# Optimization experiments

Hardware: AMD Instinct MI355X
Metric: run time of the kernel (lower is better)

The kernel has to match this reference:

```python
import jax, jax.numpy as jnp
import numpy as np

B, T, D = 4, 4096, 1024
H, HD = 16, 64
EPS = 1e-6


def setup_inputs() -> dict:
    key = jax.random.key(0)
    ks = jax.random.split(key, 5)
    scale = 1.0 / np.sqrt(D)
    return {
        "x": jax.random.normal(ks[0], (B, T, D), dtype=jnp.float32),
        "Wq": jax.random.normal(ks[1], (D, H * HD), dtype=jnp.float32) * scale,
        "Wk": jax.random.normal(ks[2], (D, H * HD), dtype=jnp.float32) * scale,
        "Wv": jax.random.normal(ks[3], (D, H * HD), dtype=jnp.float32) * scale,
        "Wo": jax.random.normal(ks[4], (H * HD, D), dtype=jnp.float32) * scale,
    }


def _feature_map(x):
    # ELU + 1 feature map (always positive)
    return jax.nn.elu(x) + 1.0


def _causal_linear_attention(q, k, v, eps=EPS):
    # q,k,v: (B,H,T,Dk/Dv) -> scan over T with running state
    Dk = q.shape[-1]
    Dv = v.shape[-1]
    qT = jnp.moveaxis(q, 2, 0)  # (T,B,H,Dk)
    kT = jnp.moveaxis(k, 2, 0)
    vT = jnp.moveaxis(v, 2, 0)

    S0 = jnp.zeros((q.shape[0], q.shape[1], Dk, Dv), dtype=q.dtype)
    z0 = jnp.zeros((q.shape[0], q.shape[1], Dk), dtype=q.dtype)

    def step(carry, qkv_t):
        S, z = carry
        q_t, k_t, v_t = qkv_t
        S = S + jnp.einsum('bhd,bhe->bhde', k_t, v_t)
        z = z + k_t
        num = jnp.einsum('bhd,bhde->bhe', q_t, S)
        den = jnp.einsum('bhd,bhd->bh', q_t, z) + eps
        return (S, z), num / den[..., None]

    _, yT = jax.lax.scan(step, (S0, z0), (qT, kT, vT))  # yT: (T,B,H,Dv)
    return jnp.moveaxis(yT, 0, 2)  # (B,H,T,Dv)


def reference(x, Wq, Wk, Wv, Wo):
    b, t, _ = x.shape

    def proj(W):
        return (x @ W).reshape(b, t, H, HD).transpose(0, 2, 1, 3)  # (B,H,T,HD)

    q = _feature_map(proj(Wq))
    k = _feature_map(proj(Wk))
    v = proj(Wv)
    y = _causal_linear_attention(q, k, v)  # (B,H,T,HD)
    y = y.transpose(0, 2, 1, 3).reshape(b, t, H * HD)
    return y @ Wo
```

## Files before the change

kernel.cpp:

```cpp
#include <hip/hip_runtime.h>


typedef __bf16 bf16;
typedef __bf16 bf16x4 __attribute__((ext_vector_type(4)));
typedef __bf16 bf16x8 __attribute__((ext_vector_type(8)));
typedef float f32x4 __attribute__((ext_vector_type(4)));

#define EPS 1e-6f

#define BAR() asm volatile("s_barrier" ::: "memory")
#define VMCNT4() asm volatile("s_waitcnt vmcnt(4)" ::: "memory")
#define VMCNT0() asm volatile("s_waitcnt vmcnt(0)" ::: "memory")

__device__ __forceinline__ void gl_lds16(const void* g, void* l) {
  __builtin_amdgcn_global_load_lds(
      (__attribute__((address_space(1))) void*)g,
      (__attribute__((address_space(3))) void*)l, 16, 0, 0);
}

__device__ __forceinline__ float fmact(float v) {
  return v > 0.f ? v + 1.f : __expf(v);
}

__global__ __launch_bounds__(256) void prep(const float* __restrict__ x,
                                            const float* __restrict__ Wq,
                                            const float* __restrict__ Wk,
                                            const float* __restrict__ Wv,
                                            const float* __restrict__ Wo,
                                            bf16* __restrict__ XB,
                                            bf16* __restrict__ WT3,
                                            bf16* __restrict__ WOT) {
  const int bid = blockIdx.x;
  const int t = threadIdx.x;
  if (bid < 8192) {
    size_t base = ((size_t)bid * 256 + t) * 8;
    float4 v0 = *(const float4*)&x[base];
    float4 v1 = *(const float4*)&x[base + 4];
    bf16x8 o;
    o[0] = (bf16)v0.x; o[1] = (bf16)v0.y; o[2] = (bf16)v0.z; o[3] = (bf16)v0.w;
    o[4] = (bf16)v1.x; o[5] = (bf16)v1.y; o[6] = (bf16)v1.z; o[7] = (bf16)v1.w;
    *(bf16x8*)&XB[base] = o;
    return;
  }
  __shared__ float tile[64][65];
  const int wi = (bid - 8192) >> 8;
  const int local = (bid - 8192) & 255;
  const float* W = (wi == 0) ? Wq : (wi == 1) ? Wk : (wi == 2) ? Wv : Wo;
  bf16* WT = (wi == 3) ? WOT : WT3 + (size_t)wi * 1048576;
  const int k0 = (local & 15) * 64, n0 = (local >> 4) * 64;
  {
    const int r4 = t / 16, c4 = (t % 16) * 4;
#pragma unroll
    for (int rr = 0; rr < 4; ++rr) {
      int r = r4 + rr * 16;
      float4 v = *(const float4*)&W[(size_t)(k0 + r) * 1024 + n0 + c4];
      tile[r][c4] = v.x; tile[r][c4 + 1] = v.y;
      tile[r][c4 + 2] = v.z; tile[r][c4 + 3] = v.w;
    }
  }
  __syncthreads();
  const int nl = t / 4, kb = (t % 4) * 16;
  bf16x8 o0, o1;
#pragma unroll
  for (int j = 0; j < 8; ++j) {
    o0[j] = (bf16)tile[kb + j][nl];
    o1[j] = (bf16)tile[kb + 8 + j][nl];
  }
  *(bf16x8*)&WT[(size_t)(n0 + nl) * 1024 + k0 + kb] = o0;
  *(bf16x8*)&WT[(size_t)(n0 + nl) * 1024 + k0 + kb + 8] = o1;
}

template <int PROJ>
__global__ __launch_bounds__(512, 2) void gemm8(const bf16* __restrict__ A,
                                                const bf16* __restrict__ BT,
                                                bf16* __restrict__ Obf,
                                                float* __restrict__ Of,
                                                const int N, const int gy) {
  extern __shared__ bf16 lds[];
  const int t = threadIdx.x;
  const int w = t >> 6, l = t & 63;
  const int nwg = (int)gridDim.x, cpx = nwg >> 3;
  const int f = ((int)blockIdx.x & 7) * cpx + ((int)blockIdx.x >> 3);
  const int bx = f / gy, by = f - bx * gy;
  const int m0 = bx * 256, n0 = by * 256;
  const int wm = (w >> 2) * 128, wn = (w & 3) * 64;
  const int lr = l & 15, lg = l >> 4;
  const int aslc = (w >> 2) * 8192;
  const int bslc = 16384 + ((w & 3) >> 1) * 8192;
  const int brow = (w & 1) * 64;
  const int srow = t >> 3;
  const int scol = ((t & 7) ^ ((t >> 3) & 7)) * 8;

  f32x4 acc[8][4] = {};
  bf16x8 bv[8];

#define FRAG(c, slc, sr_, ks_)                                          \
  (*(const bf16x8*)&lds[(c) * 32768 + (slc) + (sr_) * 64 +              \
                        (((ks_) * 32 + lg * 8) ^ (((sr_) & 7) << 3))])

#define STG(dbuf, slc, rbase, PTR, kt)                                        \
  do {                                                                        \
    const bf16* _s = (PTR) + (size_t)((rbase) + srow) * 1024 + (kt) * 64 + scol; \
    bf16* _d = lds + (dbuf) * 32768 + (slc) + w * 512;                        \
    gl_lds16(_s, _d);                                                         \
    gl_lds16(_s + 65536, _d + 4096);                                          \
  } while (0)

#define PHASE(c, q, STAGE_STMT, VM)                                           \
  {                                                                           \
    bf16x8 av[4];                                                             \
    _Pragma("unroll") for (int mi = 0; mi < 2; ++mi)                          \
      _Pragma("unroll") for (int kk = 0; kk < 2; ++kk)                        \
        av[mi * 2 + kk] = FRAG(c, aslc, (q) * 32 + mi * 16 + lr, kk);         \
    if ((q) == 0) {                                                           \
      _Pragma("unroll") for (int n = 0; n < 4; ++n)                           \
        _Pragma("unroll") for (int kk = 0; kk < 2; ++kk)                      \
          bv[n * 2 + kk] = FRAG(c, bslc, brow + n * 16 + lr, kk);             \
    }                                                                         \
    STAGE_STMT;                                                               \
    if (VM) VMCNT4();                                                         \
    BAR();                                                                    \
    __builtin_amdgcn_s_setprio(1);                                            \
    _Pragma("unroll") for (int mi = 0; mi < 2; ++mi)                          \
      _Pragma("unroll") for (int n = 0; n < 4; ++n)                           \
        _Pragma("unroll") for (int kk = 0; kk < 2; ++kk)                      \
          acc[(q) * 2 + mi][n] = __builtin_amdgcn_mfma_f32_16x16x32_bf16(     \
              av[mi * 2 + kk], bv[n * 2 + kk], acc[(q) * 2 + mi][n], 0, 0, 0);\
    __builtin_amdgcn_s_setprio(0);                                            \
    BAR();                                                                    \
  }

  STG(0, 0, m0, A, 0);        STG(0, 8192, m0 + 128, A, 0);
  STG(0, 16384, n0, BT, 0);   STG(0, 24576, n0 + 128, BT, 0);
  STG(1, 16384, n0, BT, 1);   STG(1, 24576, n0 + 128, BT, 1);
  VMCNT4();
  BAR();

#pragma unroll 1
  for (int I = 0; I < 8; ++I) {
    const int t2 = 2 * I;
    const int k1 = t2 + 1;
    const int k2 = (t2 + 2 > 15) ? 15 : t2 + 2;
    const int k3 = (t2 + 3 > 15) ? 15 : t2 + 3;
    PHASE(0, 0, STG(1, 0, m0, A, k1), 0);
    PHASE(0, 1, STG(1, 8192, m0 + 128, A, k1), 0);
    PHASE(0, 2, STG(0, 16384, n0, BT, k2), 0);
    PHASE(0, 3, STG(0, 24576, n0 + 128, BT, k2), 1);
    PHASE(1, 0, STG(0, 0, m0, A, k2), 0);
    PHASE(1, 1, STG(0, 8192, m0 + 128, A, k2), 0);
    PHASE(1, 2, STG(1, 16384, n0, BT, k3), 0);
    PHASE(1, 3, STG(1, 24576, n0 + 128, BT, k3), 1);
  }
  VMCNT0();
#undef PHASE
#undef STG
#undef FRAG
#pragma unroll
  for (int m = 0; m < 8; ++m)
#pragma unroll
    for (int n = 0; n < 4; ++n)
#pragma unroll
      for (int r = 0; r < 4; ++r) {
        int row = m0 + wm + m * 16 + lg * 4 + r;
        int col = n0 + wn + n * 16 + lr;
        float v = acc[m][n][r];
        if (PROJ) {
          if (col < 2048) v = fmact(v);
          Obf[(size_t)row * N + col] = (bf16)v;
        } else {
          Of[(size_t)row * N + col] = v;
        }
      }
}

__global__ __launch_bounds__(256) void chunk_ktv(const bf16* __restrict__ QKV,
                                                 float* __restrict__ S_ws,
                                                 float* __restrict__ z_ws) {
  const int blk = blockIdx.x;
  const int bh = blk >> 5, c = blk & 31;
  const int b = bh >> 4, h = bh & 15;
  const size_t rowbase = (size_t)b * 4096 + (size_t)c * 128;
  __shared__ alignas(16) bf16 KT[64 * 136];
  __shared__ alignas(16) bf16 VT[64 * 136];
  __shared__ float zpart[4][64];
  const int t = threadIdx.x;
  {
    const int r = t >> 1, c0 = (t & 1) * 32;
    const bf16* kp = QKV + (rowbase + r) * 3072 + 1024 + h * 64 + c0;
    const bf16* vp = QKV + (rowbase + r) * 3072 + 2048 + h * 64 + c0;
    bf16x8 kv[4], vv[4];
#pragma unroll
    for (int q8 = 0; q8 < 4; ++q8) {
      kv[q8] = *(const bf16x8*)&kp[q8 * 8];
      vv[q8] = *(const bf16x8*)&vp[q8 * 8];
    }
#pragma unroll
    for (int q8 = 0; q8 < 4; ++q8)
#pragma unroll
      for (int j = 0; j < 8; ++j) {
        KT[(c0 + q8 * 8 + j) * 136 + r] = kv[q8][j];
        VT[(c0 + q8 * 8 + j) * 136 + r] = vv[q8][j];
      }
  }
  __syncthreads();
  {
    const int d = t & 63, part = t >> 6;
    float zs = 0.f;
#pragma unroll
    for (int tt = 0; tt < 32; ++tt) zs += (float)KT[d * 136 + part * 32 + tt];
    zpart[part][d] = zs;
  }
  __syncthreads();
  if (t < 64)
    z_ws[(size_t)blk * 64 + t] =
        zpart[0][t] + zpart[1][t] + zpart[2][t] + zpart[3][t];
  const int l = t & 63, w = t >> 6;
  const int lr = l & 15, lg = l >> 4, lk = lg * 8;
  f32x4 acc[4] = {};
#pragma unroll
  for (int ks = 0; ks < 4; ++ks) {
    const int k0 = ks * 32;
    bf16x8 a = *(const bf16x8*)&VT[(w * 16 + lr) * 136 + k0 + lk];
#pragma unroll
    for (int n = 0; n < 4; ++n) {
      bf16x8 bk = *(const bf16x8*)&KT[(n * 16 + lr) * 136 + k0 + lk];
      acc[n] = __builtin_amdgcn_mfma_f32_16x16x32_bf16(a, bk, acc[n], 0, 0, 0);
    }
  }
#pragma unroll
  for (int n = 0; n < 4; ++n)
#pragma unroll
    for (int r = 0; r < 4; ++r) {
      int e = w * 16 + lg * 4 + r;
      int d = n * 16 + lr;
      S_ws[((size_t)blk * 64 + e) * 64 + d] = acc[n][r];
    }
}

__global__ __launch_bounds__(256) void prefix_scan(const float* __restrict__ S_ws,
                                                   const float* __restrict__ z_ws,
                                                   bf16* __restrict__ STp,
                                                   float* __restrict__ zP) {
  const int bh = blockIdx.x >> 2, dq = blockIdx.x & 3;
  const int t = threadIdx.x;
  const int e = t >> 2, d0 = dq * 16 + (t & 3) * 4;
  float r0 = 0.f, r1 = 0.f, r2 = 0.f, r3 = 0.f, zr = 0.f;
  const bool doz = (dq == 0) && (t < 64);
  const size_t base = (size_t)bh * 32;
  float4 v = *(const float4*)&S_ws[base * 4096 + e * 64 + d0];
  float zv = doz ? z_ws[base * 64 + t] : 0.f;
  for (int c = 0; c < 32; ++c) {
    float4 vn = {0.f, 0.f, 0.f, 0.f};
    float zn = 0.f;
    if (c < 31) {
      vn = *(const float4*)&S_ws[(base + c + 1) * 4096 + e * 64 + d0];
      if (doz) zn = z_ws[(base + c + 1) * 64 + t];
    }
    const size_t cb = base + c;
    bf16x4 o;
    o[0] = (bf16)r0; o[1] = (bf16)r1; o[2] = (bf16)r2; o[3] = (bf16)r3;
    *(bf16x4*)&STp[cb * 4096 + e * 64 + d0] = o;
    if (doz) zP[cb * 64 + t] = zr;
    r0 += v.x; r1 += v.y; r2 += v.z; r3 += v.w;
    zr += zv;
    v = vn; zv = zn;
  }
}

__global__ __launch_bounds__(256) void chunk_attn(const bf16* __restrict__ QKV,
                                                  const bf16* __restrict__ STp,
                                                  const float* __restrict__ zP,
                                                  bf16* __restrict__ Y) {
  const int blk = blockIdx.x;
  const int bh = blk >> 5, c = blk & 31;
  const int b = bh >> 4, h = bh & 15;
  const size_t cb = (size_t)bh * 32 + c;
  const size_t rowbase = (size_t)b * 4096 + (size_t)c * 128;
  const bf16* Q = QKV + rowbase * 3072 + h * 64;
  const bf16* K = QKV + rowbase * 3072 + 1024 + h * 64;
  const bf16* V = QKV + rowbase * 3072 + 2048 + h * 64;
  __shared__ alignas(16) bf16 VT[64 * 136];
  __shared__ alignas(16) bf16 P[128 * 136];
  __shared__ float den[128];
  const int t = threadIdx.x;
  {
    const int r = t >> 1, c0 = (t & 1) * 32;
    const bf16* vp = V + (size_t)r * 3072 + c0;
    bf16x8 vv[4];
#pragma unroll
    for (int q8 = 0; q8 < 4; ++q8) vv[q8] = *(const bf16x8*)&vp[q8 * 8];
#pragma unroll
    for (int q8 = 0; q8 < 4; ++q8)
#pragma unroll
      for (int j = 0; j < 8; ++j) VT[(c0 + q8 * 8 + j) * 136 + r] = vv[q8][j];
  }
  const int l = t & 63, w = t >> 6;
  const int lr = l & 15, lg = l >> 4, lk = lg * 8;
  f32x4 acc[2][4] = {};
  f32x4 accs[2][8] = {};
#pragma unroll
  for (int kq = 0; kq < 2; ++kq) {
    const int k0 = kq * 32;
    bf16x8 am[2];
#pragma unroll
    for (int m = 0; m < 2; ++m)
      am[m] = *(const bf16x8*)&Q[(size_t)(w * 32 + m * 16 + lr) * 3072 + k0 + lk];
#pragma unroll
    for (int n = 0; n < 4; ++n) {
      bf16x8 bs = *(const bf16x8*)&STp[cb * 4096 + (size_t)(n * 16 + lr) * 64 + k0 + lk];
#pragma unroll
      for (int m = 0; m < 2; ++m)
        acc[m][n] = __builtin_amdgcn_mfma_f32_16x16x32_bf16(am[m], bs, acc[m][n], 0, 0, 0);
    }
#pragma unroll
    for (int n = 0; n < 8; ++n) {
      bf16x8 bk = *(const bf16x8*)&K[(size_t)(n * 16 + lr) * 3072 + k0 + lk];
#pragma unroll
      for (int m = 0; m < 2; ++m)
        accs[m][n] = __builtin_amdgcn_mfma_f32_16x16x32_bf16(am[m], bk, accs[m][n], 0, 0, 0);
    }
  }
#pragma unroll
  for (int m = 0; m < 2; ++m)
#pragma unroll
    for (int r = 0; r < 4; ++r) {
      const int row_c = w * 32 + m * 16 + lg * 4 + r;
      float s = 0.f;
#pragma unroll
      for (int n = 0; n < 8; ++n) {
        const int col_c = n * 16 + lr;
        float v = accs[m][n][r];
        v = (col_c <= row_c) ? v : 0.f;
        accs[m][n][r] = v;
        s += v;
      }
      s += __shfl_xor(s, 1);
      s += __shfl_xor(s, 2);
      s += __shfl_xor(s, 4);
      s += __shfl_xor(s, 8);
      if (lr == 0) den[row_c] = s;
#pragma unroll
      for (int n = 0; n < 8; ++n)
        P[row_c * 136 + n * 16 + lr] = (bf16)accs[m][n][r];
    }
  __syncthreads();
  if (t < 128) {
    float s = EPS;
    const bf16* qr = Q + (size_t)t * 3072;
    const float* zp = zP + cb * 64;
#pragma unroll
    for (int d8 = 0; d8 < 64; d8 += 8) {
      bf16x8 qv = *(const bf16x8*)&qr[d8];
#pragma unroll
      for (int j = 0; j < 8; ++j) s += (float)qv[j] * zp[d8 + j];
    }
    den[t] += s;
  }
#pragma unroll
  for (int ks = 0; ks < 4; ++ks) {
    const int k0 = ks * 32;
    bf16x8 ap[2];
#pragma unroll
    for (int m = 0; m < 2; ++m)
      ap[m] = *(const bf16x8*)&P[(w * 32 + m * 16 + lr) * 136 + k0 + lk];
#pragma unroll
    for (int n = 0; n < 4; ++n) {
      bf16x8 bv = *(const bf16x8*)&VT[(n * 16 + lr) * 136 + k0 + lk];
#pragma unroll
      for (int m = 0; m < 2; ++m)
        acc[m][n] = __builtin_amdgcn_mfma_f32_16x16x32_bf16(ap[m], bv, acc[m][n], 0, 0, 0);
    }
  }
  __syncthreads();
#pragma unroll
  for (int m = 0; m < 2; ++m)
#pragma unroll
    for (int n = 0; n < 4; ++n)
#pragma unroll
      for (int r = 0; r < 4; ++r) {
        const int row_c = w * 32 + m * 16 + lg * 4 + r;
        const int col = n * 16 + lr;
        float y = acc[m][n][r] / den[row_c];
        Y[(rowbase + row_c) * 1024 + h * 64 + col] = (bf16)y;
      }
}

extern "C" void kernel_launch(void* const* d_in, const int* in_sizes, int n_in,
                              void* d_out, int out_size, void* d_ws, size_t ws_size,
                              hipStream_t stream) {
  (void)in_sizes; (void)n_in; (void)out_size; (void)ws_size;
  const float* x  = (const float*)d_in[0];
  const float* Wq = (const float*)d_in[1];
  const float* Wk = (const float*)d_in[2];
  const float* Wv = (const float*)d_in[3];
  const float* Wo = (const float*)d_in[4];
  char* ws = (char*)d_ws;
  bf16*  XB   = (bf16*)ws;
  bf16*  WT3  = (bf16*)(ws + 33554432);
  bf16*  WOT  = (bf16*)(ws + 39845888);
  bf16*  QKV  = (bf16*)(ws + 41943040);
  float* S_ws = (float*)(ws + 142606336);
  float* z_ws = (float*)(ws + 176160768);
  bf16*  STp  = (bf16*)(ws + 176685056);
  float* zP   = (float*)(ws + 193462272);
  bf16*  Y    = XB;

  {
    auto k1 = gemm8<1>; auto k0 = gemm8<0>;
    (void)hipFuncSetAttribute((const void*)k1,
        hipFuncAttributeMaxDynamicSharedMemorySize, 131072);
    (void)hipFuncSetAttribute((const void*)k0,
        hipFuncAttributeMaxDynamicSharedMemorySize, 131072);
  }

  prep<<<9216, 256, 0, stream>>>(x, Wq, Wk, Wv, Wo, XB, WT3, WOT);
  gemm8<1><<<768, 512, 131072, stream>>>(XB, WT3, QKV, nullptr, 3072, 12);
  chunk_ktv<<<2048, 256, 0, stream>>>(QKV, S_ws, z_ws);
  prefix_scan<<<256, 256, 0, stream>>>(S_ws, z_ws, STp, zP);
  chunk_attn<<<2048, 256, 0, stream>>>(QKV, STp, zP, Y);
  gemm8<0><<<256, 512, 131072, stream>>>(Y, WOT, nullptr, (float*)d_out, 1024, 4);
}
```

Baseline: 265.0 us.

## Software-pipeline LDS fragment reads one phase ahead of MFMA compute in GEMM

```diff
diff --git a/kernel.cpp b/kernel.cpp
--- a/kernel.cpp
+++ b/kernel.cpp
@@ -92,7 +92,8 @@
   const int scol = ((t & 7) ^ ((t >> 3) & 7)) * 8;
 
   f32x4 acc[8][4] = {};
-  bf16x8 bv[8];
+  bf16x8 av0[4], av1[4];
+  bf16x8 bv0[8], bv1[8];
 
 #define FRAG(c, slc, sr_, ks_)                                          \
   (*(const bf16x8*)&lds[(c) * 32768 + (slc) + (sr_) * 64 +              \
@@ -106,35 +107,32 @@
     gl_lds16(_s + 65536, _d + 4096);                                          \
   } while (0)
 
-#define PHASE(c, q, STAGE_STMT, VM)                                           \
-  {                                                                           \
-    bf16x8 av[4];                                                             \
-    _Pragma("unroll") for (int mi = 0; mi < 2; ++mi)                          \
+#define RDA(dst, c, q)                                                        \
+  _Pragma("unroll") for (int mi = 0; mi < 2; ++mi)                            \
+    _Pragma("unroll") for (int kk = 0; kk < 2; ++kk)                          \
+      dst[mi * 2 + kk] = FRAG(c, aslc, (q) * 32 + mi * 16 + lr, kk);
+
+#define RDB(dst, c)                                                           \
+  _Pragma("unroll") for (int n = 0; n < 4; ++n)                               \
+    _Pragma("unroll") for (int kk = 0; kk < 2; ++kk)                          \
+      dst[n * 2 + kk] = FRAG(c, bslc, brow + n * 16 + lr, kk);
+
+#define MM(q, av_, bv_)                                                       \
+  __builtin_amdgcn_s_setprio(1);                                              \
+  _Pragma("unroll") for (int mi = 0; mi < 2; ++mi)                            \
+    _Pragma("unroll") for (int n = 0; n < 4; ++n)                             \
       _Pragma("unroll") for (int kk = 0; kk < 2; ++kk)                        \
-        av[mi * 2 + kk] = FRAG(c, aslc, (q) * 32 + mi * 16 + lr, kk);         \
-    if ((q) == 0) {                                                           \
-      _Pragma("unroll") for (int n = 0; n < 4; ++n)                           \
-        _Pragma("unroll") for (int kk = 0; kk < 2; ++kk)                      \
-          bv[n * 2 + kk] = FRAG(c, bslc, brow + n * 16 + lr, kk);             \
-    }                                                                         \
-    STAGE_STMT;                                                               \
-    if (VM) VMCNT4();                                                         \
-    BAR();                                                                    \
-    __builtin_amdgcn_s_setprio(1);                                            \
-    _Pragma("unroll") for (int mi = 0; mi < 2; ++mi)                          \
-      _Pragma("unroll") for (int n = 0; n < 4; ++n)                           \
-        _Pragma("unroll") for (int kk = 0; kk < 2; ++kk)                      \
-          acc[(q) * 2 + mi][n] = __builtin_amdgcn_mfma_f32_16x16x32_bf16(     \
-              av[mi * 2 + kk], bv[n * 2 + kk], acc[(q) * 2 + mi][n], 0, 0, 0);\
-    __builtin_amdgcn_s_setprio(0);                                            \
-    BAR();                                                                    \
-  }
+        acc[(q) * 2 + mi][n] = __builtin_amdgcn_mfma_f32_16x16x32_bf16(       \
+            av_[mi * 2 + kk], bv_[n * 2 + kk], acc[(q) * 2 + mi][n], 0, 0, 0);\
+  __builtin_amdgcn_s_setprio(0);
 
   STG(0, 0, m0, A, 0);        STG(0, 8192, m0 + 128, A, 0);
   STG(0, 16384, n0, BT, 0);   STG(0, 24576, n0 + 128, BT, 0);
   STG(1, 16384, n0, BT, 1);   STG(1, 24576, n0 + 128, BT, 1);
   VMCNT4();
   BAR();
+  RDA(av0, 0, 0);
+  RDB(bv0, 0);
 
 #pragma unroll 1
   for (int I = 0; I < 8; ++I) {
@@ -142,17 +140,32 @@
     const int k1 = t2 + 1;
     const int k2 = (t2 + 2 > 15) ? 15 : t2 + 2;
     const int k3 = (t2 + 3 > 15) ? 15 : t2 + 3;
-    PHASE(0, 0, STG(1, 0, m0, A, k1), 0);
-    PHASE(0, 1, STG(1, 8192, m0 + 128, A, k1), 0);
-    PHASE(0, 2, STG(0, 16384, n0, BT, k2), 0);
-    PHASE(0, 3, STG(0, 24576, n0 + 128, BT, k2), 1);
-    PHASE(1, 0, STG(0, 0, m0, A, k2), 0);
-    PHASE(1, 1, STG(0, 8192, m0 + 128, A, k2), 0);
-    PHASE(1, 2, STG(1, 16384, n0, BT, k3), 0);
-    PHASE(1, 3, STG(1, 24576, n0 + 128, BT, k3), 1);
+    STG(1, 0, m0, A, k1);
+    BAR(); RDA(av1, 0, 1); MM(0, av0, bv0); BAR();
+    STG(1, 8192, m0 + 128, A, k1);
+    BAR(); RDA(av0, 0, 2); MM(1, av1, bv0); BAR();
+    STG(0, 16384, n0, BT, k2);
+    BAR(); RDA(av1, 0, 3); MM(2, av0, bv0); BAR();
+    STG(0, 24576, n0 + 128, BT, k2);
+    VMCNT4();
+    BAR(); RDA(av0, 1, 0); RDB(bv1, 1); MM(3, av1, bv0); BAR();
+    STG(0, 0, m0, A, k2);
+    BAR(); RDA(av1, 1, 1); MM(0, av0, bv1); BAR();
+    STG(0, 8192, m0 + 128, A, k2);
+    BAR(); RDA(av0, 1, 2); MM(1, av1, bv1); BAR();
+    STG(1, 16384, n0, BT, k3);
+    BAR(); RDA(av1, 1, 3); MM(2, av0, bv1); BAR();
+    STG(1, 24576, n0 + 128, BT, k3);
+    VMCNT4();
+    BAR();
+    if (I < 7) { RDA(av0, 0, 0); RDB(bv0, 0); }
+    MM(3, av1, bv1);
+    BAR();
   }
   VMCNT0();
-#undef PHASE
+#undef MM
+#undef RDB
+#undef RDA
 #undef STG
 #undef FRAG
 #pragma unroll
```

Measured after the change: 273.0 us. +3.0%, slower.
